# Kernel optimization log

Hardware: AMD Instinct MI355X
Metric: run time of the kernel (lower is better)

The kernel has to match this reference:

```python
import jax, jax.numpy as jnp
import numpy as np
import math

# ---- constants for bandwidth 32 SOFT transforms ----
NL = 32                 # bandwidth (number of degrees l)
NB = 2 * NL             # 64 samples per angle
SZ = 2 * NL - 1         # 63 centered frequencies m,n in [-31,31]
EPS = 1e-5

_lf = np.concatenate([[0.0], np.cumsum(np.log(np.arange(1, 2 * NL + 1, dtype=np.float64)))])  # log k!

def _wigner_d_dense(betas):
    """Wigner little-d d^l_{m',m}(beta), l<NL, zero padded to [nb, NL, SZ, SZ] (centered m+31)."""
    nb = len(betas)
    c = np.cos(betas / 2.0); s = np.sin(betas / 2.0)
    D = np.zeros((nb, NL, SZ, SZ), dtype=np.float64)
    for l in range(NL):
        for mp in range(-l, l + 1):
            for m in range(-l, l + 1):
                k = np.arange(max(0, m - mp), min(l + m, l - mp) + 1)
                logc = 0.5 * (_lf[l + mp] + _lf[l - mp] + _lf[l + m] + _lf[l - m]) \
                       - (_lf[l + m - k] + _lf[k] + _lf[mp - m + k] + _lf[l - mp - k])
                sign = np.where((mp - m + k) % 2 == 0, 1.0, -1.0)
                ca = 2 * l + m - mp - 2 * k   # cos(beta/2) exponent
                sb = mp - m + 2 * k           # sin(beta/2) exponent
                val = ((sign * np.exp(logc))[None, :] * c[:, None] ** ca[None, :] * s[:, None] ** sb[None, :]).sum(1)
                D[:, l, mp + NL - 1, m + NL - 1] = val
    return D

_betas = (np.arange(NB) + 0.5) / NB * np.pi
_j = np.arange(NB); _kk = np.arange(NL)
# Driscoll-Healy / SOFT quadrature weights: sum_j w_j d^l d^l' = 2/(2l+1) delta_{ll'}
_qw = (2.0 / NL) * np.sin(np.pi * (2 * _j + 1) / (4.0 * NL)) * \
      ((1.0 / (2 * _kk + 1))[None, :] * np.sin(np.outer(2 * _j + 1, 2 * _kk + 1) * np.pi / (4.0 * NL))).sum(1)

_D = _wigner_d_dense(_betas)                               # [beta, l, m, n]
_Deq = _wigner_d_dense(np.array([np.pi / 2.0]))[0]         # [l, m, n] at beta=pi/2 (equatorial grids)

WD_FWD = jnp.asarray((_qw[:, None, None, None] * _D).astype(np.float32))   # analysis weights
WD0_FWD = WD_FWD[:, :, :, NL - 1]                                           # n=0 column, for S2 fft
WD_INV = jnp.asarray((((2 * np.arange(NL) + 1) / 2.0)[None, :, None, None] * _D).astype(np.float32))
DEQ = jnp.asarray(_Deq.astype(np.float32))
D0EQ = DEQ[:, :, NL - 1]                                                     # d^l_{m,0}(pi/2)

_alphas = 2 * np.pi * np.arange(NB) / NB
PHASE = jnp.asarray(np.exp(1j * np.outer(_alphas, np.arange(-(NL - 1), NL))).astype(np.complex64))  # [p, m]

S2_SCALE = 1.0 / math.sqrt(NB * 3 * (NL ** 4) / (NL ** 2))   # 1/sqrt(len(grid)*nfi*b_out^4/b_in^2)

def _so3_scale(nfi):
    return 1.0 / math.sqrt(NB * nfi)                          # b_in == b_out -> b ratio is 1

# ---- transform helpers ----

def _centered1(xh):
    return jnp.fft.fftshift(xh, axes=-1)[..., 1:]             # drop m=-32, keep [-31,31]

def _centered2(xh):
    return jnp.fft.fftshift(xh, axes=(-2, -1))[..., 1:, 1:]

def _so3_synth(z):
    # z: [b,c,l,m,n] complex spectrum -> real SO(3) signal [b,c,beta,alpha,gamma]
    Xt = jnp.einsum('zlmn,bclmn->bczmn', WD_INV, z)
    Xp = jnp.pad(Xt, ((0, 0), (0, 0), (0, 0), (1, 0), (1, 0)))  # reinsert zero m,n=-32 bins
    x = jnp.fft.ifft2(jnp.fft.ifftshift(Xp, axes=(-2, -1)), axes=(-2, -1))
    return x.real

def _s2_conv(x, K, bias):
    # x: [b, c, beta, alpha]
    F = jnp.einsum('zlm,bczm->bclm', WD0_FWD, _centered1(jnp.fft.fft(x, axis=-1)))
    Kh = S2_SCALE * jnp.einsum('iop,pn->ion', K, jnp.conj(PHASE))   # conj kernel alpha-spectrum
    # z^l_{mn} = sum_i F^l_m(i) * conj(Y^l_n(i,o)),  Y^l_n = sum_p K_p e^{i n a_p} d^l_{n0}(pi/2)
    z = jnp.einsum('bilm,ion,ln->bolmn', F, Kh, D0EQ)
    return _so3_synth(z) + bias[None, :, None, None, None]

def _so3_conv(x, K, bias, scale):
    # x: [b, c, beta, alpha, gamma]
    F = jnp.einsum('zlmn,bczmn->bclmn', WD_FWD, _centered2(jnp.fft.fft2(x, axes=(-2, -1))))
    Kh = scale * jnp.einsum('iop,pn->ion', K, jnp.conj(PHASE))
    # z^l_{mn} = sum_{i,k} F^l_{mk}(i) * conj(Y^l_{nk}(i,o)); factorized to avoid huge dense Y
    C = jnp.einsum('bilmk,lnk->bilmn', F, DEQ)
    z = jnp.einsum('ion,bilmn->bolmn', Kh, C)
    return _so3_synth(z) + bias[None, :, None, None, None]

def _bn(x, g, b):
    mu = jnp.mean(x, axis=(0, 2, 3, 4), keepdims=True)
    var = jnp.mean((x - mu) ** 2, axis=(0, 2, 3, 4), keepdims=True)
    return (x - mu) * jax.lax.rsqrt(var + EPS) * g[None, :, None, None, None] + b[None, :, None, None, None]

def setup_inputs() -> dict:
    key = jax.random.key(0)
    ks = jax.random.split(key, 8)
    u = lambda k, shp: jax.random.uniform(k, shp, jnp.float32, -1.0, 1.0)
    return {
        'x': jax.random.normal(ks[0], (2, 3, 64, 64), jnp.float32),
        'k_s2': u(ks[1], (3, 25, 64)), 'bias_s2': jnp.zeros((25,), jnp.float32),
        'k1': u(ks[2], (25, 25, 64)), 'bias1': jnp.zeros((25,), jnp.float32),
        'k2': u(ks[3], (50, 25, 64)), 'bias2': jnp.zeros((25,), jnp.float32),
        'k3': u(ks[4], (75, 36, 64)), 'bias3': jnp.zeros((36,), jnp.float32),
        'g1': jnp.ones((25,), jnp.float32), 'b1': jnp.zeros((25,), jnp.float32),
        'g2': jnp.ones((50,), jnp.float32), 'b2': jnp.zeros((50,), jnp.float32),
        'g3': jnp.ones((75,), jnp.float32), 'b3': jnp.zeros((75,), jnp.float32),
        'g4': jnp.ones((36,), jnp.float32), 'b4': jnp.zeros((36,), jnp.float32),
    }

def reference(x, k_s2, bias_s2, k1, bias1, k2, bias2, k3, bias3,
              g1, b1, g2, b2, g3, b3, g4, b4):
    x1 = _s2_conv(x, k_s2, bias_s2)                          # [2,25,64,64,64]
    h = jax.nn.relu(_bn(x1, g1, b1))
    x2 = _so3_conv(h, k1, bias1, _so3_scale(25))             # [2,25,64,64,64]
    h = jax.nn.relu(_bn(jnp.concatenate((x1, x2), 1), g2, b2))
    x3 = _so3_conv(h, k2, bias2, _so3_scale(50))             # [2,25,64,64,64]
    h = jax.nn.relu(_bn(jnp.concatenate((x1, x2, x3), 1), g3, b3))
    h = _so3_conv(h, k3, bias3, _so3_scale(75))              # [2,36,64,64,64]
    h = jax.nn.relu(_bn(h, g4, b4))
    return jnp.mean(h, -1)                                    # integrate over gamma -> [2,36,64,64]
```

## Files before the change

### kernel.cpp

```cpp
#include <hip/hip_runtime.h>
#include <math.h>

#define PI_D 3.14159265358979323846
#define TPB 256
typedef unsigned short ushortT;
typedef unsigned int uintT;

__device__ __forceinline__ float2 cxmul(float2 a, float2 b){
  return make_float2(a.x*b.x - a.y*b.y, a.x*b.y + a.y*b.x);
}
__device__ __forceinline__ float bf2f(ushortT u){
  uintT x = ((uintT)u) << 16;
  return __uint_as_float(x);
}
__device__ __forceinline__ ushortT f2bf(float f){
  uintT x = __float_as_uint(f);
  x = x + 0x7FFFu + ((x >> 16) & 1u);
  return (ushortT)(x >> 16);
}

__global__ void k_tables(double* lf, double* qw){
  if (threadIdx.x == 0){
    lf[0] = 0.0;
    for (int i = 1; i <= 64; ++i) lf[i] = lf[i-1] + log((double)i);
  }
  int j = threadIdx.x;
  if (j < 64){
    double s1 = sin(PI_D*(2*j+1)/128.0);
    double inner = 0.0;
    for (int k = 0; k < 32; ++k)
      inner += (1.0/(double)(2*k+1)) * sin((double)(2*j+1)*(double)(2*k+1)*PI_D/128.0);
    qw[j] = (2.0/32.0) * s1 * inner;
  }
}

__device__ double wigd(const double* lfs, int l, int mp, int m, double lc, double ls){
  if (mp < -l || mp > l || m < -l || m > l) return 0.0;
  int k0 = (m - mp > 0) ? (m - mp) : 0;
  int k1 = (l + m < l - mp) ? (l + m) : (l - mp);
  double base = 0.5*(lfs[l+mp] + lfs[l-mp] + lfs[l+m] + lfs[l-m]);
  double val = 0.0;
  for (int k = k0; k <= k1; ++k){
    double t = base - lfs[l+m-k] - lfs[k] - lfs[mp-m+k] - lfs[l-mp-k]
             + (double)(2*l + m - mp - 2*k)*lc + (double)(mp - m + 2*k)*ls;
    double e = exp(t);
    val += ((mp - m + k) & 1) ? -e : e;
  }
  return val;
}

__global__ __launch_bounds__(TPB) void k_wigner(const double* __restrict__ lf,
                                                float* __restrict__ Dz2, float* __restrict__ D0,
                                                float* __restrict__ Deq){
  __shared__ double lfs[65];
  if (threadIdx.x < 65) lfs[threadIdx.x] = lf[threadIdx.x];
  __syncthreads();
  int zs = blockIdx.x, l = blockIdx.y;
  double beta = (zs < 64) ? ((double)zs + 0.5)*PI_D/64.0 : PI_D*0.5;
  double ch = cos(beta*0.5), sh = sin(beta*0.5);
  double lc = log(ch), ls = log(sh);
  if (zs < 64){
    for (int idx = threadIdx.x; idx < 2048; idx += TPB){
      int mi = idx >> 6, nf = idx & 63;
      float v = (nf < 63) ? (float)wigd(lfs, l, mi, nf-31, lc, ls) : 0.f;
      int nt = nf >> 3, nn = nf & 7;
      Dz2[(((size_t)(mi*8 + nt)*64 + zs)*32 + l)*8 + nn] = v;
      if (nf == 31) D0[((size_t)zs*32 + l)*32 + mi] = v;
    }
  } else {
    for (int idx = threadIdx.x; idx < 3969; idx += TPB){
      int r = idx/63, c = idx%63;
      Deq[((size_t)l*63 + r)*63 + c] = (float)wigd(lfs, l, r-31, c-31, lc, ls);
    }
  }
}

__global__ void k_kh(const float* __restrict__ K, float2* __restrict__ Kh, int I, int O, float scale){
  int idx = blockIdx.x*blockDim.x + threadIdx.x;
  if (idx >= I*O*63) return;
  int n = idx % 63, i = (idx/63) % I, o = idx/(63*I);
  float sr = 0.f, si = 0.f;
  for (int p = 0; p < 64; ++p){
    int t = (p * (n - 31)) & 63;
    float s, c;
    sincosf(-(float)PI_D/32.f * (float)t, &s, &c);
    float kv = K[(i*O + o)*64 + p];
    sr += kv * c; si += kv * s;
  }
  Kh[((size_t)o*I + i)*63 + n] = make_float2(sr*scale, si*scale);
}

__global__ void k_s2_fft(const float* __restrict__ x, float2* __restrict__ XH2){
  int idx = blockIdx.x*blockDim.x + threadIdx.x;
  if (idx >= 2*3*64*63) return;
  int mi = idx % 63; int z = (idx/63) & 63; int bc = idx / (63*64);
  int f = (mi + 33) & 63;
  const float* row = x + ((size_t)bc*64 + z)*64;
  float sr = 0.f, si = 0.f;
  for (int a = 0; a < 64; ++a){
    int t = (f*a) & 63;
    float s, c;
    sincosf(-(float)PI_D/32.f * (float)t, &s, &c);
    sr += row[a]*c; si += row[a]*s;
  }
  XH2[idx] = make_float2(sr, si);
}

__global__ void k_s2_F(const float* __restrict__ D0, const double* __restrict__ qw,
                       const float2* __restrict__ XH2, float2* __restrict__ F2){
  int idx = blockIdx.x*blockDim.x + threadIdx.x;
  if (idx >= 2*3*32*63) return;
  int r = idx % 63; int l = (idx/63) & 31; int bc = idx / (63*32);
  float2 acc = make_float2(0,0);
  for (int z = 0; z < 64; ++z){
    float d;
    if (r >= 31) d = D0[((size_t)z*32 + l)*32 + (r-31)];
    else {
      d = D0[((size_t)z*32 + l)*32 + (31-r)];
      if ((31-r) & 1) d = -d;
    }
    float wv = (float)qw[z] * d;
    float2 v = XH2[((size_t)bc*64 + z)*63 + r];
    acc.x += wv*v.x; acc.y += wv*v.y;
  }
  F2[idx] = acc;
}

__global__ void k_s2_zhat(const float* __restrict__ Deq, const float2* __restrict__ F2,
                          const float2* __restrict__ Kh, float2* __restrict__ Z){
  int idx = blockIdx.x*blockDim.x + threadIdx.x;
  if (idx >= 2*25*32*2016) return;
  int n = idx % 63; int mi = (idx/63) & 31; int l = (idx/2016) & 31;
  int o = (idx/(2016*32)) % 25; int b = idx/(2016*32*25);
  float deq0 = Deq[((size_t)l*63 + n)*63 + 31];
  float2 acc = make_float2(0,0);
  for (int i = 0; i < 3; ++i){
    float2 f = F2[((size_t)(b*3 + i)*32 + l)*63 + (mi+31)];
    float2 kh = Kh[((size_t)(o*3 + i))*63 + n];
    acc.x = fmaf(kh.x, f.x, acc.x); acc.x = fmaf(-kh.y, f.y, acc.x);
    acc.y = fmaf(kh.x, f.y, acc.y); acc.y = fmaf(kh.y, f.x, acc.y);
  }
  Z[((size_t)((b*25+o)*32) + l)*2016 + mi*63 + n] = make_float2(acc.x*deq0, acc.y*deq0);
}

__global__ __launch_bounds__(TPB) void k_bnstats(const ushortT* __restrict__ src, int slotBase,
                                                 double* __restrict__ part){
  int c = blockIdx.x, blk = blockIdx.y;
  const uint2* s4 = (const uint2*)src;
  double s = 0.0, q = 0.0;
  for (int k = 0; k < 8; ++k){
    int g4 = blk*2048 + k*256 + threadIdx.x;
    int b = g4 >> 16, pos4 = g4 & 65535;
    uint2 u = s4[((size_t)(b*25 + c))*65536 + pos4];
    float v0 = bf2f((ushortT)(u.x & 0xffff)), v1 = bf2f((ushortT)(u.x >> 16));
    float v2 = bf2f((ushortT)(u.y & 0xffff)), v3 = bf2f((ushortT)(u.y >> 16));
    s += (double)v0 + v1 + v2 + v3;
    q += (double)v0*v0 + (double)v1*v1 + (double)v2*v2 + (double)v3*v3;
  }
  __shared__ double sh[TPB], sh2[TPB];
  sh[threadIdx.x] = s; sh2[threadIdx.x] = q;
  __syncthreads();
  for (int o = 128; o > 0; o >>= 1){
    if (threadIdx.x < o){ sh[threadIdx.x] += sh[threadIdx.x+o]; sh2[threadIdx.x] += sh2[threadIdx.x+o]; }
    __syncthreads();
  }
  if (threadIdx.x == 0){
    part[((size_t)(slotBase + c)*64 + blk)*2 + 0] = sh[0];
    part[((size_t)(slotBase + c)*64 + blk)*2 + 1] = sh2[0];
  }
}

__global__ void k_bnfinal(const double* __restrict__ part, const float* __restrict__ g,
                          const float* __restrict__ b, float2* __restrict__ ss, int C){
  int c = blockIdx.x*blockDim.x + threadIdx.x;
  if (c >= C) return;
  double s = 0.0, q = 0.0;
  for (int k = 0; k < 64; ++k){
    s += part[((size_t)c*64 + k)*2 + 0];
    q += part[((size_t)c*64 + k)*2 + 1];
  }
  double N = 524288.0;
  double mu = s / N;
  double var = q / N - mu*mu;
  double sc = (double)g[c] / sqrt(var + 1e-5);
  ss[c] = make_float2((float)sc, (float)((double)b[c] - mu*sc));
}

__device__ __forceinline__ float2 fft64_lane(float2 x, const float2* __restrict__ Wt, int lane){
  #pragma unroll
  for (int st = 0; st < 6; ++st){
    int h = 32 >> st;
    float2 p;
    p.x = __shfl_xor(x.x, h, 64);
    p.y = __shfl_xor(x.y, h, 64);
    if (lane & h){
      float2 s = make_float2(p.x - x.x, p.y - x.y);
      x = cxmul(s, Wt[(lane & (h-1)) << st]);
    } else {
      x = make_float2(x.x + p.x, x.y + p.y);
    }
  }
  return x;
}
__device__ __forceinline__ void init_W(float2* W, float sign){
  if (threadIdx.x < 64){
    float s, c;
    sincosf(sign*(float)(2.0*PI_D/64.0)*(float)threadIdx.x, &s, &c);
    W[threadIdx.x] = make_float2(c, s);
  }
}

__global__ __launch_bounds__(TPB) void k_fft2_fwd(const ushortT* __restrict__ X1, const ushortT* __restrict__ X2,
                                                  const ushortT* __restrict__ X3, const float2* __restrict__ ss,
                                                  float2* __restrict__ XH, int Cin, int z0){
  __shared__ float2 W[64];
  __shared__ __attribute__((aligned(16))) float2 smem[4224];
  float2* bufP = smem;
  float2* bufW = smem + 2112;
  int bc = blockIdx.x, zz = blockIdx.y, z = z0 + zz;
  int b = bc / Cin, ci = bc % Cin;
  const ushortT* src; int cl;
  if (ci < 25){ src = X1; cl = ci; }
  else if (ci < 50){ src = X2; cl = ci - 25; }
  else { src = X3; cl = ci - 50; }
  src += ((size_t)(b*25 + cl)*64 + z)*4096;
  float2 sc = ss[ci];
  init_W(W, -1.f);
  int tid = threadIdx.x, lane = tid & 63, wid = tid >> 6;
  int rl = (int)(__brev((uintT)lane) >> 26);
  const uintT* s32 = (const uintT*)src;
  for (int i = tid; i < 2048; i += TPB){
    uintT u = s32[i];
    float v0 = fmaxf(bf2f((ushortT)(u & 0xffff))*sc.x + sc.y, 0.f);
    float v1 = fmaxf(bf2f((ushortT)(u >> 16))*sc.x + sc.y, 0.f);
    int a1 = i >> 5, c = i & 31;
    bufP[a1*33 + c] = make_float2(v0, v1);
  }
  __syncthreads();
  #pragma unroll 2
  for (int j = 0; j < 8; ++j){
    int c = wid*8 + j;
    float2 x = bufP[lane*33 + c];
    x = fft64_lane(x, W, lane);
    bufW[rl*33 + c] = x;
  }
  __syncthreads();
  for (int i = tid; i < 1024; i += TPB){
    int f1 = i >> 5, c = i & 31;
    float2 Wv = bufW[f1*33 + c];
    float2 Wm = bufW[((64-f1)&63)*33 + c];
    bufP[f1*65 + 2*c]     = make_float2(0.5f*(Wv.x + Wm.x), 0.5f*(Wv.y - Wm.y));
    bufP[f1*65 + 2*c + 1] = make_float2(0.5f*(Wv.y + Wm.y), 0.5f*(Wm.x - Wv.x));
  }
  __syncthreads();
  #pragma unroll 2
  for (int j = 0; j < 8; ++j){
    int r = wid*8 + j;
    float2 x = bufP[r*65 + lane];
    x = fft64_lane(x, W, lane);
    bufP[r*65 + rl] = x;
  }
  __syncthreads();
  float2* dst = XH + ((size_t)bc*32 + zz)*2016;
  for (int idx = tid; idx < 2016; idx += TPB){
    int mi = idx / 63, n = idx % 63;
    dst[idx] = bufP[mi*65 + ((n+33)&63)];
  }
}

#define SKEW(e) ((e) + ((e)>>4))
__global__ __launch_bounds__(TPB) void k_wig_F(const float* __restrict__ Dz2, const double* __restrict__ qw,
                                               const float2* __restrict__ XHa, const float2* __restrict__ XHb,
                                               float2* __restrict__ F, int BC){
  __shared__ __attribute__((aligned(16))) float sm[9088];
  float* Dt = sm;
  float2* Xt = (float2*)(sm + 4608);
  int mi = blockIdx.x, nt = blockIdx.y, bcBase = blockIdx.z*16;
  int tid = threadIdx.x;
  int bg = tid & 3, lg = (tid>>2)&7, ng = tid>>5;
  const float* DzB = Dz2 + ((size_t)(mi*8 + nt)*64)*256;
  float2 acc[4][4];
  #pragma unroll
  for (int a = 0; a < 4; ++a)
    #pragma unroll
    for (int j = 0; j < 4; ++j) acc[a][j] = make_float2(0,0);
  for (int chunk = 0; chunk < 4; ++chunk){
    const float2* XH = (chunk < 2) ? XHa : XHb;
    int zq = (chunk & 1)*16;
    int gz0 = chunk*16;
    __syncthreads();
    for (int idx = tid; idx < 4096; idx += TPB){
      int z = idx >> 8, l = (idx>>3)&31, nn = idx&7;
      float v = DzB[(size_t)gz0*256 + idx] * (float)qw[gz0+z];
      Dt[(z*8+nn)*36 + l] = v;
    }
    for (int idx = tid; idx < 2048; idx += TPB){
      int bc = idx >> 7, z = (idx>>3)&15, nn = idx&7;
      int gbc = bcBase + bc, n = nt*8 + nn;
      float2 v = make_float2(0,0);
      if (gbc < BC && n < 63) v = XH[((size_t)gbc*32 + zq + z)*2016 + mi*63 + n];
      Xt[bc*130 + z*8 + nn] = v;
    }
    __syncthreads();
    #pragma unroll 4
    for (int z = 0; z < 16; ++z){
      const float4 d = *(const float4*)&Dt[(z*8+ng)*36 + lg*4];
      float dd[4] = {d.x, d.y, d.z, d.w};
      float2 xv[4];
      #pragma unroll
      for (int j = 0; j < 4; ++j) xv[j] = Xt[(bg + 4*j)*130 + z*8 + ng];
      #pragma unroll
      for (int j = 0; j < 4; ++j)
        #pragma unroll
        for (int dl = 0; dl < 4; ++dl){
          acc[j][dl].x = fmaf(dd[dl], xv[j].x, acc[j][dl].x);
          acc[j][dl].y = fmaf(dd[dl], xv[j].y, acc[j][dl].y);
        }
    }
  }
  __syncthreads();
  float2* St = (float2*)sm;
  #pragma unroll
  for (int j = 0; j < 4; ++j)
    #pragma unroll
    for (int dl = 0; dl < 4; ++dl){
      int e = (bg + 4*j)*256 + (lg*4 + dl)*8 + ng;
      St[SKEW(e)] = acc[j][dl];
    }
  __syncthreads();
  for (int idx = tid; idx < 4096; idx += TPB){
    int bc = idx >> 8, l = (idx>>3)&31, nn = idx&7;
    int gbc = bcBase + bc, n = nt*8 + nn;
    if (gbc < BC && n < 63)
      F[((size_t)(gbc*32 + l))*2016 + mi*63 + n] = St[SKEW(idx)];
  }
}

__global__ __launch_bounds__(TPB) void k_deq_C(const float* __restrict__ Deq, const float2* __restrict__ F,
                                               float2* __restrict__ C, int BC){
  __shared__ __attribute__((aligned(16))) float sm[12604];
  float2* Fb = (float2*)sm;
  float* DeqT = sm + 8320;
  int l = blockIdx.x, mi = blockIdx.y, biBase = blockIdx.z*64;
  int tid = threadIdx.x;
  int ngr = tid & 15, big = tid >> 4;
  for (int idx = tid; idx < 3969; idx += TPB){
    int n = idx/63, k = idx - n*63;
    DeqT[k*68 + n] = Deq[((size_t)l*63 + n)*63 + k];
  }
  for (int idx = tid; idx < 4032; idx += TPB){
    int bi = idx/63, k = idx - bi*63;
    int gbi = biBase + bi;
    Fb[bi*65 + k] = (gbi < BC) ? F[((size_t)(gbi*32 + l))*2016 + mi*63 + k] : make_float2(0,0);
  }
  __syncthreads();
  float2 acc[4][4];
  #pragma unroll
  for (int a = 0; a < 4; ++a)
    #pragma unroll
    for (int j = 0; j < 4; ++j) acc[a][j] = make_float2(0,0);
  #pragma unroll 3
  for (int k = 0; k < 63; ++k){
    const float4 d = *(const float4*)&DeqT[k*68 + ngr*4];
    float dd[4] = {d.x, d.y, d.z, d.w};
    float2 fv[4];
    #pragma unroll
    for (int j = 0; j < 4; ++j) fv[j] = Fb[(big + 16*j)*65 + k];
    #pragma unroll
    for (int j = 0; j < 4; ++j)
      #pragma unroll
      for (int dn = 0; dn < 4; ++dn){
        acc[j][dn].x = fmaf(dd[dn], fv[j].x, acc[j][dn].x);
        acc[j][dn].y = fmaf(dd[dn], fv[j].y, acc[j][dn].y);
      }
  }
  __syncthreads();
  float2* St = (float2*)sm;
  #pragma unroll
  for (int j = 0; j < 4; ++j)
    #pragma unroll
    for (int dn = 0; dn < 4; ++dn){
      int n = ngr*4 + dn;
      if (n < 63) St[(big + 16*j)*63 + n] = acc[j][dn];
    }
  __syncthreads();
  for (int idx = tid; idx < 4032; idx += TPB){
    int bi = idx/63, n = idx - bi*63;
    int gbi = biBase + bi;
    if (gbi < BC) C[((size_t)(gbi*32 + l))*2016 + mi*63 + n] = St[idx];
  }
}

#define KOC 9
__global__ __launch_bounds__(TPB) void k_kh_z(const float2* __restrict__ C, const float2* __restrict__ Kh,
                                              float2* __restrict__ Z, int I, int O){
  __shared__ float2 Kt[KOC*5*64];
  const int nK = KOC*5*64;
  int l = blockIdx.x, mic = blockIdx.y, oc = blockIdx.z;
  int lane = threadIdx.x & 63, wid = threadIdx.x >> 6;
  int mi0 = mic*8 + wid*2;
  int n = lane;
  int o0 = oc*KOC;
  float2 acc[2][2][KOC];
  #pragma unroll
  for (int ml = 0; ml < 2; ++ml)
    #pragma unroll
    for (int b = 0; b < 2; ++b)
      #pragma unroll
      for (int oo = 0; oo < KOC; ++oo) acc[ml][b][oo] = make_float2(0,0);

  float2 pre[12];
  auto loadK = [&](int i0){
    #pragma unroll
    for (int t = 0; t < 12; ++t){
      int idx = threadIdx.x + t*256;
      float2 v = make_float2(0,0);
      if (idx < nK){
        int nn = idx & 63, rem = idx >> 6;
        int ic = rem % 5, oo = rem / 5;
        int o = o0 + oo;
        if (o < O && nn < 63) v = Kh[((size_t)o*I + (i0+ic))*63 + nn];
      }
      pre[t] = v;
    }
  };
  loadK(0);

  size_t cBase0 = ((size_t)l)*2016 + mi0*63 + n;
  size_t cBase1 = cBase0 + 63;
  int nch = I/5;
  for (int c = 0; c < nch; ++c){
    __syncthreads();
    #pragma unroll
    for (int t = 0; t < 12; ++t){
      int idx = threadIdx.x + t*256;
      if (idx < nK) Kt[idx] = pre[t];
    }
    __syncthreads();
    if (c+1 < nch) loadK((c+1)*5);
    if (n < 63){
      int i0 = c*5;
      float2 cv[5][4];
      #pragma unroll
      for (int ic = 0; ic < 5; ++ic){
        int i = i0 + ic;
        cv[ic][0] = C[cBase0 + (size_t)i*64512];
        cv[ic][1] = C[cBase0 + (size_t)(I + i)*64512];
        cv[ic][2] = C[cBase1 + (size_t)i*64512];
        cv[ic][3] = C[cBase1 + (size_t)(I + i)*64512];
      }
      #pragma unroll
      for (int ic = 0; ic < 5; ++ic){
        #pragma unroll
        for (int oo = 0; oo < KOC; ++oo){
          float2 kh = Kt[(oo*5 + ic)*64 + n];
          #pragma unroll
          for (int q = 0; q < 4; ++q){
            float2 cc = cv[ic][q];
            int ml = q >> 1, b = q & 1;
            acc[ml][b][oo].x = fmaf(kh.x, cc.x, acc[ml][b][oo].x);
            acc[ml][b][oo].x = fmaf(-kh.y, cc.y, acc[ml][b][oo].x);
            acc[ml][b][oo].y = fmaf(kh.x, cc.y, acc[ml][b][oo].y);
            acc[ml][b][oo].y = fmaf(kh.y, cc.x, acc[ml][b][oo].y);
          }
        }
      }
    }
  }
  if (n < 63){
    #pragma unroll
    for (int ml = 0; ml < 2; ++ml){
      size_t zBase = ((size_t)l)*2016 + (mi0 + ml)*63 + n;
      #pragma unroll
      for (int oo = 0; oo < KOC; ++oo){
        int o = o0 + oo;
        if (o < O){
          Z[zBase + (size_t)(0*O + o)*64512] = acc[ml][0][oo];
          Z[zBase + (size_t)(1*O + o)*64512] = acc[ml][1][oo];
        }
      }
    }
  }
}

__global__ __launch_bounds__(TPB) void k_wig_synth(const float* __restrict__ Dz2, const float2* __restrict__ Z,
                                                   float2* __restrict__ Xt_g, int BO){
  __shared__ __attribute__((aligned(16))) float sm[9088];
  float* Dt = sm;
  float2* Zt = (float2*)(sm + 4608);
  int mi = blockIdx.x, nt = blockIdx.y;
  int z0 = (blockIdx.z & 1)*32;
  int boBase = (blockIdx.z >> 1)*16;
  int tid = threadIdx.x;
  int bg = tid & 3, zg = (tid>>2)&7, ng = tid>>5;
  const float* DzB = Dz2 + ((size_t)(mi*8 + nt)*64)*256;
  float2 acc[4][4];
  #pragma unroll
  for (int a = 0; a < 4; ++a)
    #pragma unroll
    for (int j = 0; j < 4; ++j) acc[a][j] = make_float2(0,0);
  for (int lq = 0; lq < 32; lq += 16){
    __syncthreads();
    for (int idx = tid; idx < 4096; idx += TPB){
      int z = idx >> 7, ll = (idx>>3)&15, nn = idx&7;
      int lG = lq + ll;
      float v = DzB[(size_t)(z0+z)*256 + lG*8 + nn] * (0.5f*(float)(2*lG+1));
      Dt[(ll*8+nn)*36 + z] = v;
    }
    for (int idx = tid; idx < 2048; idx += TPB){
      int bo = idx >> 7, ll = (idx>>3)&15, nn = idx&7;
      int gbo = boBase + bo, n = nt*8 + nn;
      float2 v = make_float2(0,0);
      if (gbo < BO && n < 63) v = Z[((size_t)(gbo*32 + lq + ll))*2016 + mi*63 + n];
      Zt[bo*130 + ll*8 + nn] = v;
    }
    __syncthreads();
    #pragma unroll 4
    for (int ll = 0; ll < 16; ++ll){
      const float4 d = *(const float4*)&Dt[(ll*8+ng)*36 + zg*4];
      float dd[4] = {d.x, d.y, d.z, d.w};
      float2 zv[4];
      #pragma unroll
      for (int j = 0; j < 4; ++j) zv[j] = Zt[(bg + 4*j)*130 + ll*8 + ng];
      #pragma unroll
      for (int j = 0; j < 4; ++j)
        #pragma unroll
        for (int dz = 0; dz < 4; ++dz){
          acc[j][dz].x = fmaf(dd[dz], zv[j].x, acc[j][dz].x);
          acc[j][dz].y = fmaf(dd[dz], zv[j].y, acc[j][dz].y);
        }
    }
  }
  __syncthreads();
  float2* St = (float2*)sm;
  #pragma unroll
  for (int j = 0; j < 4; ++j)
    #pragma unroll
    for (int dz = 0; dz < 4; ++dz){
      int e = (bg + 4*j)*256 + (zg*4 + dz)*8 + ng;
      St[SKEW(e)] = acc[j][dz];
    }
  __syncthreads();
  for (int idx = tid; idx < 4096; idx += TPB){
    int bo = idx >> 8, z = (idx>>3)&31, nn = idx&7;
    int gbo = boBase + bo, n = nt*8 + nn;
    if (gbo < BO && n < 63)
      Xt_g[((size_t)gbo*64 + z0 + z)*2016 + mi*63 + n] = St[SKEW(idx)];
  }
}

__device__ __forceinline__ void inv_stage_rows(const float2* __restrict__ src, float2* bufR,
                                               const float2* W, int lane, int wid, int rl){
  int tid = threadIdx.x;
  if (tid < 64) bufR[32*65 + tid] = make_float2(0,0);
  else if (tid < 96) bufR[(tid-64)*65 + 32] = make_float2(0,0);
  for (int idx = tid; idx < 2016; idx += TPB){
    int mi = idx / 63, ni = idx - mi*63;
    bufR[mi*65 + ((ni+33)&63)] = src[idx];
  }
  __syncthreads();
  #pragma unroll 2
  for (int j = 0; j < 8; ++j){
    int r = wid*8 + j;
    float2 x = bufR[r*65 + lane];
    x = fft64_lane(x, W, lane);
    bufR[r*65 + rl] = x;
  }
  __syncthreads();
}
__device__ __forceinline__ float2 inv_col_pack(const float2* bufR, int f, int pc){
  float2 r0, r1;
  if (f <= 32){
    r0 = bufR[f*65 + 2*pc];
    r1 = bufR[f*65 + 2*pc + 1];
  } else {
    int g = 64 - f;
    float2 a = bufR[g*65 + 2*pc];
    float2 b = bufR[g*65 + 2*pc + 1];
    r0 = make_float2(a.x, -a.y);
    r1 = make_float2(b.x, -b.y);
  }
  return make_float2(r0.x - r1.y, r0.y + r1.x);
}

__global__ __launch_bounds__(TPB) void k_ifft2_sym(const float2* __restrict__ Xt, ushortT* __restrict__ Xo,
                                                   const float* __restrict__ bias, int O){
  __shared__ float2 W[64];
  __shared__ __attribute__((aligned(16))) float2 bufR[33*65];
  __shared__ uintT ldsOut[64*33];
  int bo = blockIdx.x >> 6;
  int o = bo % O;
  init_W(W, 1.f);
  int tid = threadIdx.x, lane = tid & 63, wid = tid >> 6;
  int rl = (int)(__brev((uintT)lane) >> 26);
  const float2* src = Xt + (size_t)blockIdx.x*2016;
  inv_stage_rows(src, bufR, W, lane, wid, rl);
  float bb = bias[o];
  #pragma unroll 2
  for (int j = 0; j < 8; ++j){
    int pc = wid*8 + j;
    float2 w = inv_col_pack(bufR, lane, pc);
    float2 x = fft64_lane(w, W, lane);
    ushortT u0 = f2bf(x.x*(1.f/4096.f) + bb);
    ushortT u1 = f2bf(x.y*(1.f/4096.f) + bb);
    ldsOut[rl*33 + pc] = (uintT)u0 | ((uintT)u1 << 16);
  }
  __syncthreads();
  uintT* dst = (uintT*)(Xo + (size_t)blockIdx.x*4096);
  for (int i = tid; i < 2048; i += TPB){
    int a1 = i >> 5, pc = i & 31;
    dst[i] = ldsOut[a1*33 + pc];
  }
}

__global__ __launch_bounds__(TPB) void k_stats3(const float2* __restrict__ Xt, double* __restrict__ part){
  int bo = blockIdx.x, zb = blockIdx.y;
  double s = 0.0, p = 0.0;
  for (int zz = 0; zz < 4; ++zz){
    const float2* pl = Xt + ((size_t)bo*64 + zb*4 + zz)*2016;
    for (int idx = threadIdx.x; idx < 2016; idx += TPB){
      float2 v = pl[idx];
      double q = (double)v.x*v.x + (double)v.y*v.y;
      p += (idx < 63) ? q : 2.0*q;
      if (idx == 31) s += v.x;
    }
  }
  __shared__ double sh[TPB], sh2[TPB];
  sh[threadIdx.x] = s; sh2[threadIdx.x] = p;
  __syncthreads();
  for (int o = 128; o > 0; o >>= 1){
    if (threadIdx.x < o){ sh[threadIdx.x] += sh[threadIdx.x+o]; sh2[threadIdx.x] += sh2[threadIdx.x+o]; }
    __syncthreads();
  }
  if (threadIdx.x == 0){
    part[((size_t)bo*16 + zb)*2 + 0] = sh[0];
    part[((size_t)bo*16 + zb)*2 + 1] = sh2[0];
  }
}

__global__ void k_fstat(const double* __restrict__ part, const float* __restrict__ bias,
                        const float* __restrict__ g, const float* __restrict__ bsh,
                        float2* __restrict__ ss, int O){
  int o = threadIdx.x;
  if (o >= O) return;
  double S = 0.0, P = 0.0;
  for (int b = 0; b < 2; ++b)
    for (int zb = 0; zb < 16; ++zb){
      size_t base = ((size_t)(b*O + o)*16 + zb)*2;
      S += part[base]; P += part[base+1];
    }
  P *= (1.0/4096.0);
  double N = 524288.0;
  double bi = bias[o];
  double mean = S/N + bi;
  double var = P/N + 2.0*bi*S/N + bi*bi - mean*mean;
  double sc = (double)g[o] / sqrt(var + 1e-5);
  ss[o] = make_float2((float)sc, (float)((bi - mean)*sc + (double)bsh[o]));
}

__global__ __launch_bounds__(TPB) void k_final(const float2* __restrict__ Xt, const float2* __restrict__ ss,
                                               float* __restrict__ out, int O){
  __shared__ float2 W[64];
  __shared__ __attribute__((aligned(16))) float2 bufR[33*65];
  __shared__ float s4[4*64];
  int bo = blockIdx.x >> 6;
  int o = bo % O;
  init_W(W, 1.f);
  int tid = threadIdx.x, lane = tid & 63, wid = tid >> 6;
  int rl = (int)(__brev((uintT)lane) >> 26);
  const float2* src = Xt + (size_t)blockIdx.x*2016;
  inv_stage_rows(src, bufR, W, lane, wid, rl);
  float2 sv = ss[o];
  float acc = 0.f;
  #pragma unroll 2
  for (int j = 0; j < 8; ++j){
    int pc = wid*8 + j;
    float2 w = inv_col_pack(bufR, lane, pc);
    float2 x = fft64_lane(w, W, lane);
    acc += fmaxf(fmaf(x.x*(1.f/4096.f), sv.x, sv.y), 0.f);
    acc += fmaxf(fmaf(x.y*(1.f/4096.f), sv.x, sv.y), 0.f);
  }
  s4[wid*64 + rl] = acc;
  __syncthreads();
  if (tid < 64)
    out[(size_t)blockIdx.x*64 + tid] = (s4[tid] + s4[64+tid] + s4[128+tid] + s4[192+tid]) * (1.f/64.f);
}

extern "C" void kernel_launch(void* const* d_in, const int* in_sizes, int n_in,
                              void* d_out, int out_size, void* d_ws, size_t ws_size,
                              hipStream_t stream){
  const float* x   = (const float*)d_in[0];
  const float* ks2 = (const float*)d_in[1];
  const float* bs2 = (const float*)d_in[2];
  const float* k1  = (const float*)d_in[3];
  const float* b1c = (const float*)d_in[4];
  const float* k2  = (const float*)d_in[5];
  const float* b2c = (const float*)d_in[6];
  const float* k3  = (const float*)d_in[7];
  const float* b3c = (const float*)d_in[8];
  const float* g1 = (const float*)d_in[9],  *bb1 = (const float*)d_in[10];
  const float* g2 = (const float*)d_in[11], *bb2 = (const float*)d_in[12];
  const float* g3 = (const float*)d_in[13], *bb3 = (const float*)d_in[14];
  const float* g4 = (const float*)d_in[15], *bb4 = (const float*)d_in[16];
  float* out = (float*)d_out;

  char* w = (char*)d_ws;
  size_t off = 0;
  auto take = [&](size_t bytes)->char*{
    char* p = w + off;
    off += (bytes + 255) & ~(size_t)255;
    return p;
  };
  float*  Dz2  = (float*) take(32ull*8*64*32*8*4);
  float*  D0   = (float*) take(64ull*32*32*4);
  float*  Deq  = (float*) take(32ull*63*63*4);
  double* lf   = (double*)take(65*8);
  double* qw   = (double*)take(64*8);
  double* part = (double*)take(75ull*64*2*8);
  float2* ss   = (float2*)take(75*8);
  float2* KhS2 = (float2*)take(63ull*25*3*8);
  float2* Kh1  = (float2*)take(63ull*25*25*8);
  float2* Kh2  = (float2*)take(63ull*25*50*8);
  float2* Kh3  = (float2*)take(63ull*36*75*8);
  float2* XH2  = (float2*)take(2ull*3*64*63*8);
  float2* F2   = (float2*)take(2ull*3*32*63*8);
  ushortT* X1  = (ushortT*)take(2ull*25*262144*2);
  ushortT* X2  = (ushortT*)take(2ull*25*262144*2);
  ushortT* X3  = (ushortT*)take(2ull*25*262144*2);
  float2* A    = (float2*)take(150ull*32*2016*8);
  float2* B    = (float2*)take(150ull*32*2016*8);
  if (off > ws_size) return;

  dim3 tpb(TPB);
  auto cdiv = [](long long a, long long b){ return (int)((a + b - 1) / b); };

  k_tables<<<1, 64, 0, stream>>>(lf, qw);
  k_wigner<<<dim3(65,32), tpb, 0, stream>>>(lf, Dz2, D0, Deq);
  k_kh<<<cdiv(3ll*25*63,TPB),  tpb, 0, stream>>>(ks2, KhS2, 3, 25,  (float)(1.0/sqrt(196608.0)));
  k_kh<<<cdiv(25ll*25*63,TPB), tpb, 0, stream>>>(k1,  Kh1, 25, 25, (float)(1.0/sqrt(1600.0)));
  k_kh<<<cdiv(50ll*25*63,TPB), tpb, 0, stream>>>(k2,  Kh2, 50, 25, (float)(1.0/sqrt(3200.0)));
  k_kh<<<cdiv(75ll*36*63,TPB), tpb, 0, stream>>>(k3,  Kh3, 75, 36, (float)(1.0/sqrt(4800.0)));

  k_s2_fft<<<cdiv(2ll*3*64*63,TPB), tpb, 0, stream>>>(x, XH2);
  k_s2_F<<<cdiv(2ll*3*32*63,TPB), tpb, 0, stream>>>(D0, qw, XH2, F2);
  k_s2_zhat<<<cdiv(2ll*25*32*2016,TPB), tpb, 0, stream>>>(Deq, F2, KhS2, B);
  k_wig_synth<<<dim3(32,8,2*cdiv(50,16)), tpb, 0, stream>>>(Dz2, B, A, 50);
  k_ifft2_sym<<<50*64, tpb, 0, stream>>>(A, X1, bs2, 25);
  k_bnstats<<<dim3(25,64), tpb, 0, stream>>>(X1, 0, part);

  auto so3 = [&](const ushortT* Xa, const ushortT* Xb, const ushortT* Xc, int Cin,
                 const float* g, const float* bb, const float2* Kh, int O,
                 const float* bias, ushortT* Xout, int isFinal){
    int BC = 2*Cin, BO = 2*O;
    k_bnfinal<<<1, 128, 0, stream>>>(part, g, bb, ss, Cin);
    k_fft2_fwd<<<dim3(BC,32), tpb, 0, stream>>>(Xa, Xb, Xc, ss, A, Cin, 0);
    k_fft2_fwd<<<dim3(BC,32), tpb, 0, stream>>>(Xa, Xb, Xc, ss, B, Cin, 32);
    k_wig_F<<<dim3(32,8,cdiv(BC,16)), tpb, 0, stream>>>(Dz2, qw, A, B, A, BC);
    k_deq_C<<<dim3(32,32,cdiv(BC,64)), tpb, 0, stream>>>(Deq, A, B, BC);
    k_kh_z<<<dim3(32,4,cdiv(O,KOC)), tpb, 0, stream>>>(B, Kh, A, Cin, O);
    k_wig_synth<<<dim3(32,8,2*cdiv(BO,16)), tpb, 0, stream>>>(Dz2, A, B, BO);
    if (!isFinal){
      k_ifft2_sym<<<BO*64, tpb, 0, stream>>>(B, Xout, bias, O);
    } else {
      k_stats3<<<dim3(BO,16), tpb, 0, stream>>>(B, part);
      k_fstat<<<1, 64, 0, stream>>>(part, bias, g4, bb4, ss, O);
      k_final<<<BO*64, tpb, 0, stream>>>(B, ss, out, O);
    }
  };

  so3(X1, X1, X1, 25, g1, bb1, Kh1, 25, b1c, X2, 0);
  k_bnstats<<<dim3(25,64), tpb, 0, stream>>>(X2, 25, part);
  so3(X1, X2, X2, 50, g2, bb2, Kh2, 25, b2c, X3, 0);
  k_bnstats<<<dim3(25,64), tpb, 0, stream>>>(X3, 50, part);
  so3(X1, X2, X3, 75, g3, bb3, Kh3, 36, b3c, nullptr, 1);
}
```

Measured before the change: 1.413 ms.

## Store intermediate spectral buffers as packed bf16 complex instead of float2

Intermediate spectra passed between the FFT, Wigner analysis/synthesis, kernel-multiply and inverse-FFT stages are now stored as packed bf16 pairs (4 bytes per complex) instead of float2 (8 bytes). A separate float2 buffer P keeps the Wigner-analysis coefficients in full precision, and k_deq_C now runs in place on it. The goal is to halve global memory traffic for these large intermediates in the bandwidth-bound stages. The cost is extra pack/unpack work and reduced precision in the intermediate spectra.

```diff
diff --git a/kernel.cpp b/kernel.cpp
--- a/kernel.cpp
+++ b/kernel.cpp
@@ -17,6 +17,12 @@
   uintT x = __float_as_uint(f);
   x = x + 0x7FFFu + ((x >> 16) & 1u);
   return (ushortT)(x >> 16);
+}
+__device__ __forceinline__ uintT pk2(float2 v){
+  return (uintT)f2bf(v.x) | ((uintT)f2bf(v.y) << 16);
+}
+__device__ __forceinline__ float2 up2(uintT u){
+  return make_float2(bf2f((ushortT)(u & 0xffff)), bf2f((ushortT)(u >> 16)));
 }
 
 __global__ void k_tables(double* lf, double* qw){
@@ -127,7 +133,7 @@
 }
 
 __global__ void k_s2_zhat(const float* __restrict__ Deq, const float2* __restrict__ F2,
-                          const float2* __restrict__ Kh, float2* __restrict__ Z){
+                          const float2* __restrict__ Kh, uintT* __restrict__ Z){
   int idx = blockIdx.x*blockDim.x + threadIdx.x;
   if (idx >= 2*25*32*2016) return;
   int n = idx % 63; int mi = (idx/63) & 31; int l = (idx/2016) & 31;
@@ -140,7 +146,7 @@
     acc.x = fmaf(kh.x, f.x, acc.x); acc.x = fmaf(-kh.y, f.y, acc.x);
     acc.y = fmaf(kh.x, f.y, acc.y); acc.y = fmaf(kh.y, f.x, acc.y);
   }
-  Z[((size_t)((b*25+o)*32) + l)*2016 + mi*63 + n] = make_float2(acc.x*deq0, acc.y*deq0);
+  Z[((size_t)((b*25+o)*32) + l)*2016 + mi*63 + n] = pk2(make_float2(acc.x*deq0, acc.y*deq0));
 }
 
 __global__ __launch_bounds__(TPB) void k_bnstats(const ushortT* __restrict__ src, int slotBase,
@@ -212,7 +218,7 @@
 
 __global__ __launch_bounds__(TPB) void k_fft2_fwd(const ushortT* __restrict__ X1, const ushortT* __restrict__ X2,
                                                   const ushortT* __restrict__ X3, const float2* __restrict__ ss,
-                                                  float2* __restrict__ XH, int Cin, int z0){
+                                                  uintT* __restrict__ XH, int Cin, int z0){
   __shared__ float2 W[64];
   __shared__ __attribute__((aligned(16))) float2 smem[4224];
   float2* bufP = smem;
@@ -261,16 +267,16 @@
     bufP[r*65 + rl] = x;
   }
   __syncthreads();
-  float2* dst = XH + ((size_t)bc*32 + zz)*2016;
+  uintT* dst = XH + ((size_t)bc*32 + zz)*2016;
   for (int idx = tid; idx < 2016; idx += TPB){
     int mi = idx / 63, n = idx % 63;
-    dst[idx] = bufP[mi*65 + ((n+33)&63)];
+    dst[idx] = pk2(bufP[mi*65 + ((n+33)&63)]);
   }
 }
 
 #define SKEW(e) ((e) + ((e)>>4))
 __global__ __launch_bounds__(TPB) void k_wig_F(const float* __restrict__ Dz2, const double* __restrict__ qw,
-                                               const float2* __restrict__ XHa, const float2* __restrict__ XHb,
+                                               const uintT* __restrict__ XHa, const uintT* __restrict__ XHb,
                                                float2* __restrict__ F, int BC){
   __shared__ __attribute__((aligned(16))) float sm[9088];
   float* Dt = sm;
@@ -285,20 +291,21 @@
     #pragma unroll
     for (int j = 0; j < 4; ++j) acc[a][j] = make_float2(0,0);
   for (int chunk = 0; chunk < 4; ++chunk){
-    const float2* XH = (chunk < 2) ? XHa : XHb;
+    const uintT* XH = (chunk < 2) ? XHa : XHb;
     int zq = (chunk & 1)*16;
     int gz0 = chunk*16;
     __syncthreads();
     for (int idx = tid; idx < 4096; idx += TPB){
-      int z = idx >> 8, l = (idx>>3)&31, nn = idx&7;
+      int z = idx >> 8;
       float v = DzB[(size_t)gz0*256 + idx] * (float)qw[gz0+z];
+      int l = (idx>>3)&31, nn = idx&7;
       Dt[(z*8+nn)*36 + l] = v;
     }
     for (int idx = tid; idx < 2048; idx += TPB){
       int bc = idx >> 7, z = (idx>>3)&15, nn = idx&7;
       int gbc = bcBase + bc, n = nt*8 + nn;
       float2 v = make_float2(0,0);
-      if (gbc < BC && n < 63) v = XH[((size_t)gbc*32 + zq + z)*2016 + mi*63 + n];
+      if (gbc < BC && n < 63) v = up2(XH[((size_t)gbc*32 + zq + z)*2016 + mi*63 + n]);
       Xt[bc*130 + z*8 + nn] = v;
     }
     __syncthreads();
@@ -393,7 +400,7 @@
 
 #define KOC 9
 __global__ __launch_bounds__(TPB) void k_kh_z(const float2* __restrict__ C, const float2* __restrict__ Kh,
-                                              float2* __restrict__ Z, int I, int O){
+                                              uintT* __restrict__ Z, int I, int O){
   __shared__ float2 Kt[KOC*5*64];
   const int nK = KOC*5*64;
   int l = blockIdx.x, mic = blockIdx.y, oc = blockIdx.z;
@@ -475,16 +482,16 @@
       for (int oo = 0; oo < KOC; ++oo){
         int o = o0 + oo;
         if (o < O){
-          Z[zBase + (size_t)(0*O + o)*64512] = acc[ml][0][oo];
-          Z[zBase + (size_t)(1*O + o)*64512] = acc[ml][1][oo];
+          Z[zBase + (size_t)(0*O + o)*64512] = pk2(acc[ml][0][oo]);
+          Z[zBase + (size_t)(1*O + o)*64512] = pk2(acc[ml][1][oo]);
         }
       }
     }
   }
 }
 
-__global__ __launch_bounds__(TPB) void k_wig_synth(const float* __restrict__ Dz2, const float2* __restrict__ Z,
-                                                   float2* __restrict__ Xt_g, int BO){
+__global__ __launch_bounds__(TPB) void k_wig_synth(const float* __restrict__ Dz2, const uintT* __restrict__ Z,
+                                                   uintT* __restrict__ Xt_g, int BO){
   __shared__ __attribute__((aligned(16))) float sm[9088];
   float* Dt = sm;
   float2* Zt = (float2*)(sm + 4608);
@@ -511,7 +518,7 @@
       int bo = idx >> 7, ll = (idx>>3)&15, nn = idx&7;
       int gbo = boBase + bo, n = nt*8 + nn;
       float2 v = make_float2(0,0);
-      if (gbo < BO && n < 63) v = Z[((size_t)(gbo*32 + lq + ll))*2016 + mi*63 + n];
+      if (gbo < BO && n < 63) v = up2(Z[((size_t)(gbo*32 + lq + ll))*2016 + mi*63 + n]);
       Zt[bo*130 + ll*8 + nn] = v;
     }
     __syncthreads();
@@ -545,18 +552,18 @@
     int bo = idx >> 8, z = (idx>>3)&31, nn = idx&7;
     int gbo = boBase + bo, n = nt*8 + nn;
     if (gbo < BO && n < 63)
-      Xt_g[((size_t)gbo*64 + z0 + z)*2016 + mi*63 + n] = St[SKEW(idx)];
-  }
-}
-
-__device__ __forceinline__ void inv_stage_rows(const float2* __restrict__ src, float2* bufR,
+      Xt_g[((size_t)gbo*64 + z0 + z)*2016 + mi*63 + n] = pk2(St[SKEW(idx)]);
+  }
+}
+
+__device__ __forceinline__ void inv_stage_rows(const uintT* __restrict__ src, float2* bufR,
                                                const float2* W, int lane, int wid, int rl){
   int tid = threadIdx.x;
   if (tid < 64) bufR[32*65 + tid] = make_float2(0,0);
   else if (tid < 96) bufR[(tid-64)*65 + 32] = make_float2(0,0);
   for (int idx = tid; idx < 2016; idx += TPB){
     int mi = idx / 63, ni = idx - mi*63;
-    bufR[mi*65 + ((ni+33)&63)] = src[idx];
+    bufR[mi*65 + ((ni+33)&63)] = up2(src[idx]);
   }
   __syncthreads();
   #pragma unroll 2
@@ -583,7 +590,7 @@
   return make_float2(r0.x - r1.y, r0.y + r1.x);
 }
 
-__global__ __launch_bounds__(TPB) void k_ifft2_sym(const float2* __restrict__ Xt, ushortT* __restrict__ Xo,
+__global__ __launch_bounds__(TPB) void k_ifft2_sym(const uintT* __restrict__ Xt, ushortT* __restrict__ Xo,
                                                    const float* __restrict__ bias, int O){
   __shared__ float2 W[64];
   __shared__ __attribute__((aligned(16))) float2 bufR[33*65];
@@ -593,7 +600,7 @@
   init_W(W, 1.f);
   int tid = threadIdx.x, lane = tid & 63, wid = tid >> 6;
   int rl = (int)(__brev((uintT)lane) >> 26);
-  const float2* src = Xt + (size_t)blockIdx.x*2016;
+  const uintT* src = Xt + (size_t)blockIdx.x*2016;
   inv_stage_rows(src, bufR, W, lane, wid, rl);
   float bb = bias[o];
   #pragma unroll 2
@@ -613,13 +620,13 @@
   }
 }
 
-__global__ __launch_bounds__(TPB) void k_stats3(const float2* __restrict__ Xt, double* __restrict__ part){
+__global__ __launch_bounds__(TPB) void k_stats3(const uintT* __restrict__ Xt, double* __restrict__ part){
   int bo = blockIdx.x, zb = blockIdx.y;
   double s = 0.0, p = 0.0;
   for (int zz = 0; zz < 4; ++zz){
-    const float2* pl = Xt + ((size_t)bo*64 + zb*4 + zz)*2016;
+    const uintT* pl = Xt + ((size_t)bo*64 + zb*4 + zz)*2016;
     for (int idx = threadIdx.x; idx < 2016; idx += TPB){
-      float2 v = pl[idx];
+      float2 v = up2(pl[idx]);
       double q = (double)v.x*v.x + (double)v.y*v.y;
       p += (idx < 63) ? q : 2.0*q;
       if (idx == 31) s += v.x;
@@ -658,7 +665,7 @@
   ss[o] = make_float2((float)sc, (float)((bi - mean)*sc + (double)bsh[o]));
 }
 
-__global__ __launch_bounds__(TPB) void k_final(const float2* __restrict__ Xt, const float2* __restrict__ ss,
+__global__ __launch_bounds__(TPB) void k_final(const uintT* __restrict__ Xt, const float2* __restrict__ ss,
                                                float* __restrict__ out, int O){
   __shared__ float2 W[64];
   __shared__ __attribute__((aligned(16))) float2 bufR[33*65];
@@ -668,7 +675,7 @@
   init_W(W, 1.f);
   int tid = threadIdx.x, lane = tid & 63, wid = tid >> 6;
   int rl = (int)(__brev((uintT)lane) >> 26);
-  const float2* src = Xt + (size_t)blockIdx.x*2016;
+  const uintT* src = Xt + (size_t)blockIdx.x*2016;
   inv_stage_rows(src, bufR, W, lane, wid, rl);
   float2 sv = ss[o];
   float acc = 0.f;
@@ -727,8 +734,9 @@
   ushortT* X1  = (ushortT*)take(2ull*25*262144*2);
   ushortT* X2  = (ushortT*)take(2ull*25*262144*2);
   ushortT* X3  = (ushortT*)take(2ull*25*262144*2);
-  float2* A    = (float2*)take(150ull*32*2016*8);
-  float2* B    = (float2*)take(150ull*32*2016*8);
+  uintT*  Ah   = (uintT*) take(150ull*32*2016*4);
+  uintT*  Bh   = (uintT*) take(150ull*32*2016*4);
+  float2* P    = (float2*)take(150ull*32*2016*8);
   if (off > ws_size) return;
 
   dim3 tpb(TPB);
@@ -743,9 +751,9 @@
 
   k_s2_fft<<<cdiv(2ll*3*64*63,TPB), tpb, 0, stream>>>(x, XH2);
   k_s2_F<<<cdiv(2ll*3*32*63,TPB), tpb, 0, stream>>>(D0, qw, XH2, F2);
-  k_s2_zhat<<<cdiv(2ll*25*32*2016,TPB), tpb, 0, stream>>>(Deq, F2, KhS2, B);
-  k_wig_synth<<<dim3(32,8,2*cdiv(50,16)), tpb, 0, stream>>>(Dz2, B, A, 50);
-  k_ifft2_sym<<<50*64, tpb, 0, stream>>>(A, X1, bs2, 25);
+  k_s2_zhat<<<cdiv(2ll*25*32*2016,TPB), tpb, 0, stream>>>(Deq, F2, KhS2, Ah);
+  k_wig_synth<<<dim3(32,8,2*cdiv(50,16)), tpb, 0, stream>>>(Dz2, Ah, Bh, 50);
+  k_ifft2_sym<<<50*64, tpb, 0, stream>>>(Bh, X1, bs2, 25);
   k_bnstats<<<dim3(25,64), tpb, 0, stream>>>(X1, 0, part);
 
   auto so3 = [&](const ushortT* Xa, const ushortT* Xb, const ushortT* Xc, int Cin,
@@ -753,18 +761,18 @@
                  const float* bias, ushortT* Xout, int isFinal){
     int BC = 2*Cin, BO = 2*O;
     k_bnfinal<<<1, 128, 0, stream>>>(part, g, bb, ss, Cin);
-    k_fft2_fwd<<<dim3(BC,32), tpb, 0, stream>>>(Xa, Xb, Xc, ss, A, Cin, 0);
-    k_fft2_fwd<<<dim3(BC,32), tpb, 0, stream>>>(Xa, Xb, Xc, ss, B, Cin, 32);
-    k_wig_F<<<dim3(32,8,cdiv(BC,16)), tpb, 0, stream>>>(Dz2, qw, A, B, A, BC);
-    k_deq_C<<<dim3(32,32,cdiv(BC,64)), tpb, 0, stream>>>(Deq, A, B, BC);
-    k_kh_z<<<dim3(32,4,cdiv(O,KOC)), tpb, 0, stream>>>(B, Kh, A, Cin, O);
-    k_wig_synth<<<dim3(32,8,2*cdiv(BO,16)), tpb, 0, stream>>>(Dz2, A, B, BO);
+    k_fft2_fwd<<<dim3(BC,32), tpb, 0, stream>>>(Xa, Xb, Xc, ss, Ah, Cin, 0);
+    k_fft2_fwd<<<dim3(BC,32), tpb, 0, stream>>>(Xa, Xb, Xc, ss, Bh, Cin, 32);
+    k_wig_F<<<dim3(32,8,cdiv(BC,16)), tpb, 0, stream>>>(Dz2, qw, Ah, Bh, P, BC);
+    k_deq_C<<<dim3(32,32,cdiv(BC,64)), tpb, 0, stream>>>(Deq, P, P, BC);
+    k_kh_z<<<dim3(32,4,cdiv(O,KOC)), tpb, 0, stream>>>(P, Kh, Ah, Cin, O);
+    k_wig_synth<<<dim3(32,8,2*cdiv(BO,16)), tpb, 0, stream>>>(Dz2, Ah, Bh, BO);
     if (!isFinal){
-      k_ifft2_sym<<<BO*64, tpb, 0, stream>>>(B, Xout, bias, O);
+      k_ifft2_sym<<<BO*64, tpb, 0, stream>>>(Bh, Xout, bias, O);
     } else {
-      k_stats3<<<dim3(BO,16), tpb, 0, stream>>>(B, part);
+      k_stats3<<<dim3(BO,16), tpb, 0, stream>>>(Bh, part);
       k_fstat<<<1, 64, 0, stream>>>(part, bias, g4, bb4, ss, O);
-      k_final<<<BO*64, tpb, 0, stream>>>(B, ss, out, O);
+      k_final<<<BO*64, tpb, 0, stream>>>(Bh, ss, out, O);
     }
   };
 
```

After: 1.399 ms. Within noise of the previous version (-1.0%).
